# Kernel tuning notes

Hardware: AMD Instinct MI355X
Metric: run time of the kernel (lower is better)

## Reference

```python
import jax, jax.numpy as jnp
import numpy as np

N = 20000   # nodes per type per hop
E = 200000  # edges per relation per hop
H = 512     # node_feature_hid_len
FU = 512    # raw user feature len
FI = 256    # raw item feature len
NUM_RES = 2
NUM_DNN = 2


def setup_inputs() -> dict:
    key = jax.random.key(0)
    ks = iter(jax.random.split(key, 64))
    p = lambda shape: jax.random.normal(next(ks), shape, dtype=jnp.float32) * 0.05
    inp = {}
    # features per hop per type
    for h in range(3):
        inp[f'feat_user_h{h}'] = jax.random.normal(next(ks), (N, FU), dtype=jnp.float32)
        inp[f'feat_item_h{h}'] = jax.random.normal(next(ks), (N, FI), dtype=jnp.float32)
    del inp['feat_user_h2_']; 


def _unused():
    pass

# rebuild setup_inputs cleanly (above stub replaced)

def setup_inputs() -> dict:
    key = jax.random.key(0)
    ks = iter(jax.random.split(key, 64))
    p = lambda shape: jax.random.normal(next(ks), shape, dtype=jnp.float32) * 0.05
    inp = {}
    for h in range(3):
        inp[f'feat_user_h{h}'] = jax.random.normal(next(ks), (N, FU), dtype=jnp.float32)
        inp[f'feat_item_h{h}'] = jax.random.normal(next(ks), (N, FI), dtype=jnp.float32)
    for name in ('edges_UI_h0', 'edges_IU_h0', 'edges_UI_h1', 'edges_IU_h1'):
        inp[name] = jax.random.randint(next(ks), (2, E), 0, N, dtype=jnp.int32)
    # per-node-type input transforms
    inp['W_user'] = p((FU, H)); inp['b_user'] = jnp.zeros((H,), jnp.float32)
    inp['W_item'] = p((FI, H)); inp['b_item'] = jnp.zeros((H,), jnp.float32)
    # per-relation GATConv params, stacked over 2 relations [UI, IU]
    inp['gat_feat_W'] = p((2, H, H)); inp['gat_feat_b'] = jnp.zeros((2, H), jnp.float32)
    inp['gat_att_w'] = p((2, 2 * H)); inp['gat_att_b'] = jnp.zeros((2,), jnp.float32)
    inp['gat_bias'] = jnp.zeros((2, H), jnp.float32)
    # Res_DNN params
    inp['prep_W'] = p((H, H)); inp['prep_b'] = jnp.zeros((H,), jnp.float32)
    inp['dnn_W'] = p((NUM_RES, NUM_DNN, H, H)); inp['dnn_b'] = jnp.zeros((NUM_RES, NUM_DNN, H), jnp.float32)
    inp['dnn_ln_g'] = jnp.ones((NUM_RES, NUM_DNN, H), jnp.float32); inp['dnn_ln_b'] = jnp.zeros((NUM_RES, NUM_DNN, H), jnp.float32)
    inp['res_ln_g'] = jnp.ones((NUM_RES, H), jnp.float32); inp['res_ln_b'] = jnp.zeros((NUM_RES, H), jnp.float32)
    inp['cls_W'] = p((H, 1)); inp['cls_b'] = jnp.zeros((1,), jnp.float32)
    return inp


def _ln(x, g, b, eps=1e-5):
    mu = jnp.mean(x, axis=-1, keepdims=True)
    var = jnp.mean((x - mu) ** 2, axis=-1, keepdims=True)
    return (x - mu) * jax.lax.rsqrt(var + eps) * g + b


def _gat(head_h, tail_h, edges, fW, fb, aw, ab, bias):
    # GATConv: feat_linear on both sides, tanh edge attention, per-source-row
    # sparse softmax, scatter-weighted sum of transformed tail features.
    s = head_h @ fW + fb            # [Nh, H]
    t = tail_h @ fW + fb            # [Nt, H]
    src, tgt = edges[0], edges[1]
    # att(cat([s_e, t_e])) split into per-node scores (same math as concat @ aw)
    e = jnp.tanh((s @ aw[:H])[src] + (t @ aw[H:])[tgt] + ab)  # [E]
    nh = head_h.shape[0]
    m = jax.ops.segment_max(e, src, num_segments=nh)
    ex = jnp.exp(e - m[src])
    den = jax.ops.segment_sum(ex, src, num_segments=nh)
    alpha = ex / den[src]
    hp = jax.ops.segment_sum(alpha[:, None] * t[tgt], src, num_segments=nh)
    return hp + bias


def _forward(feat_user_h0, feat_item_h0, feat_user_h1, feat_item_h1,
             feat_user_h2, feat_item_h2,
             W_user, b_user, W_item, b_item,
             gat_feat_W, gat_feat_b, gat_att_w, gat_att_b, gat_bias,
             prep_W, prep_b, dnn_W, dnn_b, dnn_ln_g, dnn_ln_b,
             res_ln_g, res_ln_b, cls_W, cls_b,
             edges_UI_h0, edges_IU_h0, edges_UI_h1, edges_IU_h1):
    def gat(r, head, tail, edges):
        return _gat(head, tail, edges, gat_feat_W[r], gat_feat_b[r],
                    gat_att_w[r], gat_att_b[r], gat_bias[r])
    # hop 2 (deepest): transformed source features
    su = feat_user_h2 @ W_user + b_user
    si = feat_item_h2 @ W_item + b_item
    # hop 1
    hu = feat_user_h1 @ W_user + b_user
    hi = feat_item_h1 @ W_item + b_item
    su_new = (hu + gat(0, hu, si, edges_UI_h1)) * 0.5  # mean of [self, UI agg]
    si_new = (hi + gat(1, hi, su, edges_IU_h1)) * 0.5
    su, si = su_new, si_new
    # hop 0
    hu = feat_user_h0 @ W_user + b_user
    hi = feat_item_h0 @ W_item + b_item
    su_new = (hu + gat(0, hu, si, edges_UI_h0)) * 0.5
    su = su_new  # target node type = 'user' (first key)
    # Res_DNN head
    x = su @ prep_W + prep_b
    for r in range(NUM_RES):
        sc = x
        for d in range(NUM_DNN):
            x = _ln(jnp.tanh(x @ dnn_W[r, d] + dnn_b[r, d]), dnn_ln_g[r, d], dnn_ln_b[r, d])
        x = _ln(jnp.tanh(sc + x), res_ln_g[r], res_ln_b[r])
    return jax.nn.sigmoid(x @ cls_W + cls_b)  # [N, 1]


def reference(feat_user_h0, feat_item_h0, feat_user_h1, feat_item_h1,
              feat_user_h2, feat_item_h2,
              edges_UI_h0, edges_IU_h0, edges_UI_h1, edges_IU_h1,
              W_user, b_user, W_item, b_item,
              gat_feat_W, gat_feat_b, gat_att_w, gat_att_b, gat_bias,
              prep_W, prep_b, dnn_W, dnn_b, dnn_ln_g, dnn_ln_b,
              res_ln_g, res_ln_b, cls_W, cls_b):
    return _forward(feat_user_h0, feat_item_h0, feat_user_h1, feat_item_h1,
                    feat_user_h2, feat_item_h2,
                    W_user, b_user, W_item, b_item,
                    gat_feat_W, gat_feat_b, gat_att_w, gat_att_b, gat_bias,
                    prep_W, prep_b, dnn_W, dnn_b, dnn_ln_g, dnn_ln_b,
                    res_ln_g, res_ln_b, cls_W, cls_b,
                    edges_UI_h0, edges_IU_h0, edges_UI_h1, edges_IU_h1)
```

## Files before the change

kernel.cpp:

```cpp
#include <hip/hip_runtime.h>
#include <math.h>

#define NN 20000
#define NE 200000
#define HH 512

typedef __attribute__((ext_vector_type(8))) short short8v;
typedef __attribute__((ext_vector_type(4))) float f32x4;

__device__ inline short f2bf(float f) {
    union { float f; unsigned u; } v; v.f = f;
    unsigned r = (v.u + 0x7fffu + ((v.u >> 16) & 1u)) >> 16;
    return (short)r;
}
__device__ inline float bf2f(short s) {
    union { unsigned u; float f; } v;
    v.u = ((unsigned)(unsigned short)s) << 16;
    return v.f;
}

__device__ inline void gload_lds16(const void* g, void* l) {
    __builtin_amdgcn_global_load_lds(
        (const __attribute__((address_space(1))) void*)g,
        (__attribute__((address_space(3))) void*)l, 16, 0, 0);
}

__global__ __launch_bounds__(256)
void f2b_kernel(const float* __restrict__ src, short* __restrict__ dst, int n8)
{
    int i = blockIdx.x * 256 + threadIdx.x;
    if (i >= n8) return;
    const float4* p = (const float4*)src + (size_t)i * 2;
    float4 a = p[0], b = p[1];
    short8v s;
    s[0] = f2bf(a.x); s[1] = f2bf(a.y); s[2] = f2bf(a.z); s[3] = f2bf(a.w);
    s[4] = f2bf(b.x); s[5] = f2bf(b.y); s[6] = f2bf(b.z); s[7] = f2bf(b.w);
    ((short8v*)dst)[i] = s;
}

__global__ __launch_bounds__(256)
void wtr_kernel(const float* __restrict__ src, short* __restrict__ dst,
                int K, int Ncols)
{
    __shared__ float t[32][33];
    int bx = blockIdx.x * 32;
    int by = blockIdx.y * 32;
    int tx = threadIdx.x, ty = threadIdx.y;
    for (int i = ty; i < 32; i += 8)
        t[i][tx] = src[(size_t)(by + i) * Ncols + bx + tx];
    __syncthreads();
    for (int i = ty; i < 32; i += 8)
        dst[(size_t)(bx + i) * K + by + tx] = f2bf(t[tx][i]);
}

__global__ __launch_bounds__(256)
void mfma_lin(const short* __restrict__ X, const short* __restrict__ WT,
              const float* __restrict__ bias, float* __restrict__ outF,
              short* __restrict__ outB, int M, int K)
{
    __shared__ short8v As[2][512];
    __shared__ short8v Bs[2][512];

    const int tid = threadIdx.x;
    const int lane = tid & 63;
    const int w = tid >> 6;

    const int nby = (M + 127) >> 7;
    const int nwg = nby << 2;
    const int q = nwg >> 3, r = nwg & 7;
    int id = blockIdx.x;
    int xcd = id & 7, wi = id >> 3;
    int wgid = (xcd < r ? xcd * (q + 1) : r * (q + 1) + (xcd - r) * q) + wi;
    const int col0 = (wgid & 3) * 128;
    const int row0 = (wgid >> 2) * 128;

    const int wr = (w >> 1) * 64;
    const int wc = (w & 1) * 64;

    int sp0 = w * 128 + lane;
    int sp1 = sp0 + 64;
    int r0_ = sp0 >> 2, r1_ = sp1 >> 2;
    int c0_ = (sp0 & 3) ^ ((r0_ >> 1) & 3);
    int c1_ = (sp1 & 3) ^ ((r1_ >> 1) & 3);
    int ga0 = row0 + r0_; if (ga0 >= M) ga0 = M - 1;
    int ga1 = row0 + r1_; if (ga1 >= M) ga1 = M - 1;
    const short* ag0 = X + (size_t)ga0 * K + c0_ * 8;
    const short* ag1 = X + (size_t)ga1 * K + c1_ * 8;
    const short* bg0 = WT + (size_t)(col0 + r0_) * K + c0_ * 8;
    const short* bg1 = WT + (size_t)(col0 + r1_) * K + c1_ * 8;

    int ar[4], br[4];
#pragma unroll
    for (int i = 0; i < 4; ++i) {
        int rr = wr + i * 16 + (lane & 15);
        ar[i] = rr * 4 + ((lane >> 4) ^ ((rr >> 1) & 3));
        int nn = wc + i * 16 + (lane & 15);
        br[i] = nn * 4 + ((lane >> 4) ^ ((nn >> 1) & 3));
    }

    f32x4 acc[4][4];
#pragma unroll
    for (int i = 0; i < 4; ++i)
#pragma unroll
        for (int j = 0; j < 4; ++j)
            acc[i][j] = (f32x4){0.f, 0.f, 0.f, 0.f};

    auto stage = [&](int buf, int kk) {
        gload_lds16(ag0 + kk, &As[buf][sp0 & ~63]);
        gload_lds16(ag1 + kk, &As[buf][sp1 & ~63]);
        gload_lds16(bg0 + kk, &Bs[buf][sp0 & ~63]);
        gload_lds16(bg1 + kk, &Bs[buf][sp1 & ~63]);
    };

    const int nt = K >> 5;
    stage(0, 0);
    __syncthreads();
    int cur = 0;
    for (int t = 0; t < nt; ++t) {
        if (t + 1 < nt) stage(cur ^ 1, (t + 1) * 32);
        short8v af[4], bf[4];
#pragma unroll
        for (int i = 0; i < 4; ++i) af[i] = As[cur][ar[i]];
#pragma unroll
        for (int j = 0; j < 4; ++j) bf[j] = Bs[cur][br[j]];
#pragma unroll
        for (int i = 0; i < 4; ++i)
#pragma unroll
            for (int j = 0; j < 4; ++j)
                acc[i][j] = __builtin_amdgcn_mfma_f32_16x16x32_bf16(af[i], bf[j], acc[i][j], 0, 0, 0);
        __syncthreads();
        cur ^= 1;
    }

    float bj[4];
#pragma unroll
    for (int j = 0; j < 4; ++j)
        bj[j] = bias[col0 + wc + j * 16 + (lane & 15)];
#pragma unroll
    for (int i = 0; i < 4; ++i) {
#pragma unroll
        for (int rr = 0; rr < 4; ++rr) {
            int row = row0 + wr + i * 16 + (lane >> 4) * 4 + rr;
            if (row < M) {
                size_t base = (size_t)row * HH + col0 + wc + (lane & 15);
                if (outF) {
                    float* op = outF + base;
#pragma unroll
                    for (int j = 0; j < 4; ++j) op[j * 16] = acc[i][j][rr] + bj[j];
                }
                if (outB) {
                    short* op = outB + base;
#pragma unroll
                    for (int j = 0; j < 4; ++j) op[j * 16] = f2bf(acc[i][j][rr] + bj[j]);
                }
            }
        }
    }
}

__global__ __launch_bounds__(256)
void gat_pre_kernel(const float* __restrict__ fW, const float* __restrict__ fb,
                    const float* __restrict__ aw, float* __restrict__ uv,
                    float* __restrict__ s0t0)
{
    int row = blockIdx.x * 4 + (threadIdx.x >> 6);
    int lane = threadIdx.x & 63;
    const float4* ah = (const float4*)aw;
    const float4* at = (const float4*)(aw + HH);
    const float4* fp;
    if (row < 512)      fp = (const float4*)(fW + (size_t)row * HH);
    else if (row == 512) fp = (const float4*)fb;
    else return;
    float du = 0.f, dv = 0.f;
#pragma unroll
    for (int l = 0; l < 2; ++l) {
        int idx = lane * 2 + l;
        float4 f = fp[idx], a = ah[idx], b = at[idx];
        du += f.x*a.x + f.y*a.y + f.z*a.z + f.w*a.w;
        dv += f.x*b.x + f.y*b.y + f.z*b.z + f.w*b.w;
    }
#pragma unroll
    for (int m = 32; m >= 1; m >>= 1) {
        du += __shfl_xor(du, m);
        dv += __shfl_xor(dv, m);
    }
    if (lane == 0) {
        if (row < 512) { uv[row] = du; uv[512 + row] = dv; }
        else           { s0t0[0] = du; s0t0[1] = dv; }
    }
}

__global__ __launch_bounds__(256)
void rowdot2_kernel(const short* __restrict__ Hd, const short* __restrict__ Tl,
                    const float* __restrict__ uv, const float* __restrict__ s0t0,
                    float* __restrict__ ss, float* __restrict__ ts, int N)
{
    int row = blockIdx.x * 4 + (threadIdx.x >> 6);
    int lane = threadIdx.x & 63;
    if (row >= N) return;
    short8v h = ((const short8v*)(Hd + (size_t)row * HH))[lane];
    short8v t = ((const short8v*)(Tl + (size_t)row * HH))[lane];
    const float4* up = (const float4*)uv + lane * 2;
    const float4* vp = (const float4*)(uv + HH) + lane * 2;
    float4 u0 = up[0], u1 = up[1], v0 = vp[0], v1 = vp[1];
    float a = bf2f(h[0])*u0.x + bf2f(h[1])*u0.y + bf2f(h[2])*u0.z + bf2f(h[3])*u0.w
            + bf2f(h[4])*u1.x + bf2f(h[5])*u1.y + bf2f(h[6])*u1.z + bf2f(h[7])*u1.w;
    float b = bf2f(t[0])*v0.x + bf2f(t[1])*v0.y + bf2f(t[2])*v0.z + bf2f(t[3])*v0.w
            + bf2f(t[4])*v1.x + bf2f(t[5])*v1.y + bf2f(t[6])*v1.z + bf2f(t[7])*v1.w;
#pragma unroll
    for (int m = 32; m >= 1; m >>= 1) {
        a += __shfl_xor(a, m);
        b += __shfl_xor(b, m);
    }
    if (lane == 0) { ss[row] = a + s0t0[0]; ts[row] = b + s0t0[1]; }
}

__global__ __launch_bounds__(256)
void count2_kernel(const int* __restrict__ s0, const int* __restrict__ s1,
                   int* __restrict__ c0, int* __restrict__ c1, int E)
{
    int i = blockIdx.x * blockDim.x + threadIdx.x;
    if (i < E) atomicAdd(&c0[s0[i]], 1);
    else if (i < 2 * E) atomicAdd(&c1[s1[i - E]], 1);
}

__global__ __launch_bounds__(1024)
void scan2_kernel(const int* __restrict__ c0, const int* __restrict__ c1,
                  int* __restrict__ o0, int* __restrict__ o1,
                  int* __restrict__ u0, int* __restrict__ u1, int n)
{
    const int* counts = blockIdx.x ? c1 : c0;
    int* offs = blockIdx.x ? o1 : o0;
    int* curs = blockIdx.x ? u1 : u0;
    __shared__ int part[1024];
    const int tid = threadIdx.x;
    const int CH = (n + 1023) / 1024;
    const int base = tid * CH;
    int s = 0;
    for (int i = 0; i < CH; ++i) {
        int idx = base + i;
        if (idx < n) s += counts[idx];
    }
    part[tid] = s;
    __syncthreads();
    for (int d = 1; d < 1024; d <<= 1) {
        int v = 0;
        if (tid >= d) v = part[tid - d];
        __syncthreads();
        if (tid >= d) part[tid] += v;
        __syncthreads();
    }
    int run = (tid == 0) ? 0 : part[tid - 1];
    for (int i = 0; i < CH; ++i) {
        int idx = base + i;
        if (idx < n) { offs[idx] = run; curs[idx] = run; run += counts[idx]; }
    }
    if (tid == 1023) offs[n] = run;
}

__global__ __launch_bounds__(256)
void fill_kernel(const int* __restrict__ src, const int* __restrict__ tgt,
                 const float* __restrict__ ss, const float* __restrict__ ts,
                 const float* __restrict__ ab_ptr, int* __restrict__ cursor,
                 int* __restrict__ tvals, float* __restrict__ wv, int E)
{
    int i = blockIdx.x * blockDim.x + threadIdx.x;
    if (i >= E) return;
    int s = src[i], t = tgt[i];
    int pos = atomicAdd(&cursor[s], 1);
    tvals[pos] = t;
    wv[pos] = expf(tanhf(ss[s] + ts[t] + ab_ptr[0]));
}

__global__ __launch_bounds__(256)
void gat_agg_kernel(const int* __restrict__ offs, const int* __restrict__ tvals,
                    const float* __restrict__ wv, const short* __restrict__ T,
                    const short* __restrict__ head, const float* __restrict__ gbias,
                    short* __restrict__ out, int N)
{
    int s = blockIdx.x * 4 + (threadIdx.x >> 6);
    int lane = threadIdx.x & 63;
    if (s >= N) return;
    const int beg = offs[s], end = offs[s + 1];
    float a[8];
#pragma unroll
    for (int q = 0; q < 8; ++q) a[q] = 0.f;
    float den = 0.f;

    int j = beg;
    float wq = 0.f; short8v tvq;
    if (j < end) {
        wq = wv[j];
        tvq = ((const short8v*)(T + (size_t)tvals[j] * HH))[lane];
    }
    while (j < end) {
        float w = wq; short8v tv = tvq;
        ++j;
        if (j < end) {
            wq = wv[j];
            tvq = ((const short8v*)(T + (size_t)tvals[j] * HH))[lane];
        }
        den += w;
#pragma unroll
        for (int q = 0; q < 8; ++q) a[q] = fmaf(w, bf2f(tv[q]), a[q]);
    }
    float inv = (den > 0.f) ? 1.f / den : 0.f;

    short8v h = ((const short8v*)(head + (size_t)s * HH))[lane];
    const float4* bp = (const float4*)gbias + lane * 2;
    float4 b0 = bp[0], b1 = bp[1];
    float bb[8] = {b0.x, b0.y, b0.z, b0.w, b1.x, b1.y, b1.z, b1.w};
    short8v o;
#pragma unroll
    for (int q = 0; q < 8; ++q)
        o[q] = f2bf((bf2f(h[q]) + a[q] * inv + bb[q]) * 0.5f);
    ((short8v*)(out + (size_t)s * HH))[lane] = o;
}

__global__ __launch_bounds__(256)
void tanh_ln_kernel(const short* __restrict__ Z, const float* __restrict__ res,
                    const float* __restrict__ g, const float* __restrict__ bta,
                    short* __restrict__ outB, float* __restrict__ outF,
                    const float* __restrict__ cWp, const float* __restrict__ cbp,
                    float* __restrict__ outCls, int N)
{
    int row = blockIdx.x * 4 + (threadIdx.x >> 6);
    int lane = threadIdx.x & 63;
    if (row >= N) return;
    short8v zv = ((const short8v*)(Z + (size_t)row * HH))[lane];
    float v[8];
    float sum = 0.f, sum2 = 0.f;
    float rr[8];
    if (res) {
        const float4* rp = (const float4*)(res + (size_t)row * HH) + lane * 2;
        float4 r0 = rp[0], r1 = rp[1];
        rr[0]=r0.x; rr[1]=r0.y; rr[2]=r0.z; rr[3]=r0.w;
        rr[4]=r1.x; rr[5]=r1.y; rr[6]=r1.z; rr[7]=r1.w;
    } else {
#pragma unroll
        for (int q = 0; q < 8; ++q) rr[q] = 0.f;
    }
#pragma unroll
    for (int q = 0; q < 8; ++q) {
        float t = tanhf(bf2f(zv[q]) + rr[q]);
        v[q] = t;
        sum += t;
        sum2 = fmaf(t, t, sum2);
    }
#pragma unroll
    for (int m = 32; m >= 1; m >>= 1) {
        sum  += __shfl_xor(sum, m);
        sum2 += __shfl_xor(sum2, m);
    }
    float mu  = sum * (1.f/HH);
    float var = sum2 * (1.f/HH) - mu*mu;
    float rs  = rsqrtf(var + 1e-5f);
    const float4* gp = (const float4*)g + lane * 2;
    const float4* bp = (const float4*)bta + lane * 2;
    float4 g0 = gp[0], g1 = gp[1], c0 = bp[0], c1 = bp[1];
    float gg[8] = {g0.x, g0.y, g0.z, g0.w, g1.x, g1.y, g1.z, g1.w};
    float cc[8] = {c0.x, c0.y, c0.z, c0.w, c1.x, c1.y, c1.z, c1.w};
    float o[8];
#pragma unroll
    for (int q = 0; q < 8; ++q) o[q] = (v[q]-mu)*rs*gg[q] + cc[q];
    if (outB) {
        short8v ob;
#pragma unroll
        for (int q = 0; q < 8; ++q) ob[q] = f2bf(o[q]);
        ((short8v*)(outB + (size_t)row * HH))[lane] = ob;
    }
    if (outF) {
        float4* op = (float4*)(outF + (size_t)row * HH) + lane * 2;
        op[0] = make_float4(o[0], o[1], o[2], o[3]);
        op[1] = make_float4(o[4], o[5], o[6], o[7]);
    }
    if (cWp) {
        const float4* wp = (const float4*)cWp + lane * 2;
        float4 w0 = wp[0], w1 = wp[1];
        float acc = o[0]*w0.x + o[1]*w0.y + o[2]*w0.z + o[3]*w0.w
                  + o[4]*w1.x + o[5]*w1.y + o[6]*w1.z + o[7]*w1.w;
#pragma unroll
        for (int m = 32; m >= 1; m >>= 1) acc += __shfl_xor(acc, m);
        if (lane == 0) outCls[row] = 1.f / (1.f + expf(-(acc + cbp[0])));
    }
}

extern "C" void kernel_launch(void* const* d_in, const int* in_sizes, int n_in,
                              void* d_out, int out_size, void* d_ws, size_t ws_size,
                              hipStream_t stream)
{
    (void)in_sizes; (void)n_in; (void)out_size; (void)ws_size;
    const int N = NN, E = NE, H = HH;
    const size_t NHf = (size_t)N * H;

    const float* fu0 = (const float*)d_in[0];
    const float* fi1 = (const float*)d_in[3];
    const float* fu2 = (const float*)d_in[4];
    const int* eUI0 = (const int*)d_in[6];
    const int* eIU1 = (const int*)d_in[9];
    const float* Wu  = (const float*)d_in[10];
    const float* bu  = (const float*)d_in[11];
    const float* Wi  = (const float*)d_in[12];
    const float* bi  = (const float*)d_in[13];
    const float* gfW = (const float*)d_in[14];
    const float* gfb = (const float*)d_in[15];
    const float* gaw = (const float*)d_in[16];
    const float* gab = (const float*)d_in[17];
    const float* gbias = (const float*)d_in[18];
    const float* prW = (const float*)d_in[19];
    const float* prb = (const float*)d_in[20];
    const float* dW  = (const float*)d_in[21];
    const float* db  = (const float*)d_in[22];
    const float* dlg = (const float*)d_in[23];
    const float* dlb = (const float*)d_in[24];
    const float* rlg = (const float*)d_in[25];
    const float* rlb = (const float*)d_in[26];
    const float* cW  = (const float*)d_in[27];
    const float* cb  = (const float*)d_in[28];

    float* B5   = (float*)d_ws;
    float* ssb  = B5 + NHf;
    float* tsb  = ssb + N;
    float* uv   = tsb + N;
    float* s0t0 = uv + 1024;
    float* wvb  = s0t0 + 4;
    int* counts0 = (int*)(wvb + E);
    int* counts1 = counts0 + N;
    int* offs0   = counts1 + N;
    int* offs1   = offs0 + N + 1;
    int* cur0    = offs1 + N + 1;
    int* cur1    = cur0 + N;
    int* tvals   = cur1 + N;
    size_t boff = (size_t)((char*)(tvals + E) - (char*)d_ws);
    boff = (boff + 15) & ~(size_t)15;
    short* S0    = (short*)((char*)d_ws + boff);
    short* XI1   = S0 + NHf;
    short* SU    = XI1 + NHf / 2;
    short* HI    = SU + NHf;
    short* SINEW = HI + NHf;
    short* T4    = SINEW + NHf;
    short* SUF   = T4 + NHf;
    short* WTu   = SUF + NHf;
    short* WTi   = WTu + 512 * 512;
    short* WTg0  = WTi + 512 * 256;
    short* WTg1  = WTg0 + 512 * 512;
    short* WTpr  = WTg1 + 512 * 512;
    short* WTd   = WTpr + 512 * 512;
    short* XU0 = S0;
    short* HU0 = HI;
    short* XB  = SINEW;
    short* ZB  = SU;

    auto WTR = [&](const float* src, short* dst, int K) {
        hipLaunchKernelGGL(wtr_kernel, dim3(16, K / 32), dim3(32, 8), 0, stream,
                           src, dst, K, 512);
    };
    WTR(Wu, WTu, 512);
    WTR(Wi, WTi, 256);
    WTR(gfW, WTg0, 512);
    WTR(gfW + (size_t)H * H, WTg1, 512);
    WTR(prW, WTpr, 512);
    for (int k = 0; k < 4; ++k)
        WTR(dW + (size_t)k * H * H, WTd + (size_t)k * 512 * 512, 512);

    auto F2B = [&](const float* src, short* dst, size_t n) {
        int n8 = (int)(n / 8);
        hipLaunchKernelGGL(f2b_kernel, dim3((n8 + 255) / 256), dim3(256), 0, stream,
                           src, dst, n8);
    };

    hipMemsetAsync(counts0, 0, 2 * N * sizeof(int), stream);
    hipLaunchKernelGGL(count2_kernel, dim3((2 * E + 255) / 256), dim3(256), 0, stream,
                       eUI0, eIU1, counts0, counts1, E);
    hipLaunchKernelGGL(scan2_kernel, dim3(2), dim3(1024), 0, stream,
                       counts0, counts1, offs0, offs1, cur0, cur1, N);

    const int nby = (N + 127) / 128;
    const int nwg = nby * 4;
    auto MLIN = [&](const short* X, const short* WT, const float* b,
                    float* oF, short* oB, int K) {
        hipLaunchKernelGGL(mfma_lin, dim3(nwg), dim3(256), 0, stream,
                           X, WT, b, oF, oB, N, K);
    };
    const int rgrid = (N + 3) / 4;
    const int egrid = (E + 255) / 256;

    auto GAT = [&](int r, const short* headB, const short* tailB, const short* WTg,
                   const int* edges, int* offs, int* curs, short* outB) {
        hipLaunchKernelGGL(gat_pre_kernel, dim3(130), dim3(256), 0, stream,
                           gfW + (size_t)r * H * H, gfb + r * H, gaw + (size_t)r * 2 * H,
                           uv, s0t0);
        MLIN(tailB, WTg, gfb + r * H, nullptr, T4, 512);
        hipLaunchKernelGGL(rowdot2_kernel, dim3(rgrid), dim3(256), 0, stream,
                           headB, tailB, uv, s0t0, ssb, tsb, N);
        hipLaunchKernelGGL(fill_kernel, dim3(egrid), dim3(256), 0, stream,
                           edges, edges + E, ssb, tsb, gab + r, curs, tvals, wvb, E);
        hipLaunchKernelGGL(gat_agg_kernel, dim3(rgrid), dim3(256), 0, stream,
                           offs, tvals, wvb, T4, headB, gbias + (size_t)r * H, outB, N);
    };

    F2B(fu2, S0, NHf);
    F2B(fi1, XI1, NHf / 2);
    MLIN(S0, WTu, bu, nullptr, SU, 512);
    MLIN(XI1, WTi, bi, nullptr, HI, 256);
    GAT(1, HI, SU, WTg1, eIU1, offs1, cur1, SINEW);
    F2B(fu0, XU0, NHf);
    MLIN(XU0, WTu, bu, nullptr, HU0, 512);
    GAT(0, HU0, SINEW, WTg0, eUI0, offs0, cur0, SUF);

    MLIN(SUF, WTpr, prb, B5, XB, 512);
    for (int r = 0; r < 2; ++r) {
        for (int d = 0; d < 2; ++d) {
            MLIN(XB, WTd + (size_t)(r * 2 + d) * 512 * 512, db + (r * 2 + d) * H,
                 nullptr, ZB, 512);
            hipLaunchKernelGGL(tanh_ln_kernel, dim3(rgrid), dim3(256), 0, stream,
                               ZB, (const float*)nullptr, dlg + (r * 2 + d) * H,
                               dlb + (r * 2 + d) * H, XB, (float*)nullptr,
                               (const float*)nullptr, (const float*)nullptr,
                               (float*)nullptr, N);
        }
        if (r == 0) {
            hipLaunchKernelGGL(tanh_ln_kernel, dim3(rgrid), dim3(256), 0, stream,
                               XB, B5, rlg, rlb, XB, B5,
                               (const float*)nullptr, (const float*)nullptr,
                               (float*)nullptr, N);
        } else {
            hipLaunchKernelGGL(tanh_ln_kernel, dim3(rgrid), dim3(256), 0, stream,
                               XB, B5, rlg + H, rlb + H, (short*)nullptr,
                               (float*)nullptr, cW, cb, (float*)d_out, N);
        }
    }
}
```

Baseline: 594.7 us.

## Fuse DNN GEMMs with tanh/layernorm epilogues, batch user transforms, unroll GAT aggregation

Adds an MFMA kernel computing a full 512-wide row tile of 32 rows, so the tanh, layernorm, residual tanh-layernorm and final classifier sigmoid are applied in the epilogue instead of separate elementwise kernels. The two user feature transforms share one GEMM over 2N rows, and the GAT aggregation loop issues four gathers per iteration. This removes intermediate bf16 round trips and several launches, but the small 32-row tile reloads the whole weight matrix per block, reducing operand reuse.

Result: slower. 719.8 us (+21.0%).

```diff
diff --git a/kernel.cpp b/kernel.cpp
--- a/kernel.cpp
+++ b/kernel.cpp
@@ -154,6 +154,280 @@
                     for (int j = 0; j < 4; ++j) op[j * 16] = f2bf(acc[i][j][rr] + bj[j]);
                 }
             }
+        }
+    }
+}
+
+__global__ __launch_bounds__(256)
+void mfma_dnn(const short* __restrict__ X, const short* __restrict__ WT,
+              const float* __restrict__ bias,
+              const float* __restrict__ g1, const float* __restrict__ b1,
+              const float* __restrict__ scp,
+              const float* __restrict__ g2, const float* __restrict__ b2,
+              short* __restrict__ outB, float* __restrict__ outF,
+              const float* __restrict__ cWp, const float* __restrict__ cbp,
+              float* __restrict__ outCls, int M)
+{
+    __shared__ short8v As[128];
+    __shared__ short8v Bs[2048];
+    __shared__ float red[4][32][2];
+    __shared__ float lnp[32][2];
+
+    const int tid = threadIdx.x;
+    const int lane = tid & 63;
+    const int w = tid >> 6;
+
+    const int nwg = M >> 5;
+    const int q = nwg >> 3, r = nwg & 7;
+    int id = blockIdx.x;
+    int xcd = id & 7, wi = id >> 3;
+    int wgid = (xcd < r ? xcd * (q + 1) : r * (q + 1) + (xcd - r) * q) + wi;
+    const int row0 = wgid * 32;
+
+    const int bslotbase = w * 512;
+    const short* bgp[8];
+#pragma unroll
+    for (int g = 0; g < 8; ++g) {
+        int p = bslotbase + g * 64 + lane;
+        int col = p >> 2;
+        int ch = (p & 3) ^ ((col >> 1) & 3);
+        bgp[g] = WT + (size_t)col * HH + ch * 8;
+    }
+    const short* agp[2];
+    if (w == 0) {
+#pragma unroll
+        for (int g = 0; g < 2; ++g) {
+            int p = g * 64 + lane;
+            int row = p >> 2;
+            int ch = (p & 3) ^ ((row >> 1) & 3);
+            agp[g] = X + (size_t)(row0 + row) * HH + ch * 8;
+        }
+    }
+
+    int afr[2], bfr[8];
+#pragma unroll
+    for (int i = 0; i < 2; ++i) {
+        int rw = i * 16 + (lane & 15);
+        afr[i] = rw * 4 + ((lane >> 4) ^ ((rw >> 1) & 3));
+    }
+#pragma unroll
+    for (int j = 0; j < 8; ++j) {
+        int cc = w * 128 + j * 16 + (lane & 15);
+        bfr[j] = cc * 4 + ((lane >> 4) ^ ((cc >> 1) & 3));
+    }
+
+    f32x4 acc[2][8];
+#pragma unroll
+    for (int i = 0; i < 2; ++i)
+#pragma unroll
+        for (int j = 0; j < 8; ++j)
+            acc[i][j] = (f32x4){0.f, 0.f, 0.f, 0.f};
+
+    for (int t = 0; t < 16; ++t) {
+        int kk = t * 32;
+#pragma unroll
+        for (int g = 0; g < 8; ++g)
+            gload_lds16(bgp[g] + kk, &Bs[bslotbase + g * 64]);
+        if (w == 0) {
+#pragma unroll
+            for (int g = 0; g < 2; ++g)
+                gload_lds16(agp[g] + kk, &As[g * 64]);
+        }
+        __syncthreads();
+        short8v af[2], bf[8];
+#pragma unroll
+        for (int i = 0; i < 2; ++i) af[i] = As[afr[i]];
+#pragma unroll
+        for (int j = 0; j < 8; ++j) bf[j] = Bs[bfr[j]];
+#pragma unroll
+        for (int i = 0; i < 2; ++i)
+#pragma unroll
+            for (int j = 0; j < 8; ++j)
+                acc[i][j] = __builtin_amdgcn_mfma_f32_16x16x32_bf16(af[i], bf[j], acc[i][j], 0, 0, 0);
+        __syncthreads();
+    }
+
+    const int colb = w * 128 + (lane & 15);
+    float bj[8], g1j[8], b1j[8];
+#pragma unroll
+    for (int j = 0; j < 8; ++j) {
+        bj[j]  = bias[colb + j * 16];
+        g1j[j] = g1[colb + j * 16];
+        b1j[j] = b1[colb + j * 16];
+    }
+#pragma unroll
+    for (int i = 0; i < 2; ++i)
+#pragma unroll
+        for (int j = 0; j < 8; ++j)
+#pragma unroll
+            for (int rr = 0; rr < 4; ++rr)
+                acc[i][j][rr] = tanhf(acc[i][j][rr] + bj[j]);
+
+    {
+        float s1[2][4], s2[2][4];
+#pragma unroll
+        for (int i = 0; i < 2; ++i)
+#pragma unroll
+            for (int rr = 0; rr < 4; ++rr) {
+                float s = 0.f, ss = 0.f;
+#pragma unroll
+                for (int j = 0; j < 8; ++j) {
+                    float v = acc[i][j][rr];
+                    s += v; ss = fmaf(v, v, ss);
+                }
+#pragma unroll
+                for (int m = 1; m <= 8; m <<= 1) {
+                    s += __shfl_xor(s, m); ss += __shfl_xor(ss, m);
+                }
+                s1[i][rr] = s; s2[i][rr] = ss;
+            }
+        if ((lane & 15) == 0) {
+#pragma unroll
+            for (int i = 0; i < 2; ++i)
+#pragma unroll
+                for (int rr = 0; rr < 4; ++rr) {
+                    int row = i * 16 + (lane >> 4) * 4 + rr;
+                    red[w][row][0] = s1[i][rr];
+                    red[w][row][1] = s2[i][rr];
+                }
+        }
+        __syncthreads();
+        if (tid < 32) {
+            float s = red[0][tid][0] + red[1][tid][0] + red[2][tid][0] + red[3][tid][0];
+            float ss = red[0][tid][1] + red[1][tid][1] + red[2][tid][1] + red[3][tid][1];
+            float mu = s * (1.f / HH);
+            float var = ss * (1.f / HH) - mu * mu;
+            lnp[tid][0] = mu; lnp[tid][1] = rsqrtf(var + 1e-5f);
+        }
+        __syncthreads();
+    }
+#pragma unroll
+    for (int i = 0; i < 2; ++i)
+#pragma unroll
+        for (int rr = 0; rr < 4; ++rr) {
+            int row = i * 16 + (lane >> 4) * 4 + rr;
+            float mu = lnp[row][0], rs = lnp[row][1];
+#pragma unroll
+            for (int j = 0; j < 8; ++j)
+                acc[i][j][rr] = (acc[i][j][rr] - mu) * rs * g1j[j] + b1j[j];
+        }
+
+    if (scp) {
+#pragma unroll
+        for (int i = 0; i < 2; ++i)
+#pragma unroll
+            for (int rr = 0; rr < 4; ++rr) {
+                int row = i * 16 + (lane >> 4) * 4 + rr;
+                const float* sp = scp + (size_t)(row0 + row) * HH;
+#pragma unroll
+                for (int j = 0; j < 8; ++j)
+                    acc[i][j][rr] = tanhf(sp[colb + j * 16] + acc[i][j][rr]);
+            }
+        __syncthreads();
+        float s1[2][4], s2[2][4];
+#pragma unroll
+        for (int i = 0; i < 2; ++i)
+#pragma unroll
+            for (int rr = 0; rr < 4; ++rr) {
+                float s = 0.f, ss = 0.f;
+#pragma unroll
+                for (int j = 0; j < 8; ++j) {
+                    float v = acc[i][j][rr];
+                    s += v; ss = fmaf(v, v, ss);
+                }
+#pragma unroll
+                for (int m = 1; m <= 8; m <<= 1) {
+                    s += __shfl_xor(s, m); ss += __shfl_xor(ss, m);
+                }
+                s1[i][rr] = s; s2[i][rr] = ss;
+            }
+        if ((lane & 15) == 0) {
+#pragma unroll
+            for (int i = 0; i < 2; ++i)
+#pragma unroll
+                for (int rr = 0; rr < 4; ++rr) {
+                    int row = i * 16 + (lane >> 4) * 4 + rr;
+                    red[w][row][0] = s1[i][rr];
+                    red[w][row][1] = s2[i][rr];
+                }
+        }
+        __syncthreads();
+        if (tid < 32) {
+            float s = red[0][tid][0] + red[1][tid][0] + red[2][tid][0] + red[3][tid][0];
+            float ss = red[0][tid][1] + red[1][tid][1] + red[2][tid][1] + red[3][tid][1];
+            float mu = s * (1.f / HH);
+            float var = ss * (1.f / HH) - mu * mu;
+            lnp[tid][0] = mu; lnp[tid][1] = rsqrtf(var + 1e-5f);
+        }
+        __syncthreads();
+        float g2j[8], b2j[8];
+#pragma unroll
+        for (int j = 0; j < 8; ++j) {
+            g2j[j] = g2[colb + j * 16];
+            b2j[j] = b2[colb + j * 16];
+        }
+#pragma unroll
+        for (int i = 0; i < 2; ++i)
+#pragma unroll
+            for (int rr = 0; rr < 4; ++rr) {
+                int row = i * 16 + (lane >> 4) * 4 + rr;
+                float mu = lnp[row][0], rs = lnp[row][1];
+#pragma unroll
+                for (int j = 0; j < 8; ++j)
+                    acc[i][j][rr] = (acc[i][j][rr] - mu) * rs * g2j[j] + b2j[j];
+            }
+    }
+
+    if (outB) {
+#pragma unroll
+        for (int i = 0; i < 2; ++i)
+#pragma unroll
+            for (int rr = 0; rr < 4; ++rr) {
+                int row = row0 + i * 16 + (lane >> 4) * 4 + rr;
+                short* op = outB + (size_t)row * HH + colb;
+#pragma unroll
+                for (int j = 0; j < 8; ++j) op[j * 16] = f2bf(acc[i][j][rr]);
+            }
+    }
+    if (outF) {
+#pragma unroll
+        for (int i = 0; i < 2; ++i)
+#pragma unroll
+            for (int rr = 0; rr < 4; ++rr) {
+                int row = row0 + i * 16 + (lane >> 4) * 4 + rr;
+                float* op = outF + (size_t)row * HH + colb;
+#pragma unroll
+                for (int j = 0; j < 8; ++j) op[j * 16] = acc[i][j][rr];
+            }
+    }
+    if (cWp) {
+        float cw[8];
+#pragma unroll
+        for (int j = 0; j < 8; ++j) cw[j] = cWp[colb + j * 16];
+        __syncthreads();
+        float d[2][4];
+#pragma unroll
+        for (int i = 0; i < 2; ++i)
+#pragma unroll
+            for (int rr = 0; rr < 4; ++rr) {
+                float s = 0.f;
+#pragma unroll
+                for (int j = 0; j < 8; ++j) s = fmaf(acc[i][j][rr], cw[j], s);
+#pragma unroll
+                for (int m = 1; m <= 8; m <<= 1) s += __shfl_xor(s, m);
+                d[i][rr] = s;
+            }
+        if ((lane & 15) == 0) {
+#pragma unroll
+            for (int i = 0; i < 2; ++i)
+#pragma unroll
+                for (int rr = 0; rr < 4; ++rr)
+                    red[w][i * 16 + (lane >> 4) * 4 + rr][0] = d[i][rr];
+        }
+        __syncthreads();
+        if (tid < 32) {
+            float s = red[0][tid][0] + red[1][tid][0] + red[2][tid][0] + red[3][tid][0];
+            outCls[row0 + tid] = 1.f / (1.f + expf(-(s + cbp[0])));
         }
     }
 }
@@ -288,18 +562,28 @@
     float den = 0.f;
 
     int j = beg;
-    float wq = 0.f; short8v tvq;
-    if (j < end) {
-        wq = wv[j];
-        tvq = ((const short8v*)(T + (size_t)tvals[j] * HH))[lane];
-    }
-    while (j < end) {
-        float w = wq; short8v tv = tvq;
-        ++j;
-        if (j < end) {
-            wq = wv[j];
-            tvq = ((const short8v*)(T + (size_t)tvals[j] * HH))[lane];
-        }
+    for (; j + 4 <= end; j += 4) {
+        int t0 = tvals[j], t1 = tvals[j + 1], t2 = tvals[j + 2], t3 = tvals[j + 3];
+        float w0 = wv[j], w1 = wv[j + 1], w2 = wv[j + 2], w3 = wv[j + 3];
+        short8v v0 = ((const short8v*)(T + (size_t)t0 * HH))[lane];
+        short8v v1 = ((const short8v*)(T + (size_t)t1 * HH))[lane];
+        short8v v2 = ((const short8v*)(T + (size_t)t2 * HH))[lane];
+        short8v v3 = ((const short8v*)(T + (size_t)t3 * HH))[lane];
+        den += w0 + w1 + w2 + w3;
+#pragma unroll
+        for (int q = 0; q < 8; ++q) {
+            float acc = a[q];
+            acc = fmaf(w0, bf2f(v0[q]), acc);
+            acc = fmaf(w1, bf2f(v1[q]), acc);
+            acc = fmaf(w2, bf2f(v2[q]), acc);
+            acc = fmaf(w3, bf2f(v3[q]), acc);
+            a[q] = acc;
+        }
+    }
+    for (; j < end; ++j) {
+        int t = tvals[j];
+        float w = wv[j];
+        short8v tv = ((const short8v*)(T + (size_t)t * HH))[lane];
         den += w;
 #pragma unroll
         for (int q = 0; q < 8; ++q) a[q] = fmaf(w, bf2f(tv[q]), a[q]);
@@ -315,74 +599,6 @@
     for (int q = 0; q < 8; ++q)
         o[q] = f2bf((bf2f(h[q]) + a[q] * inv + bb[q]) * 0.5f);
     ((short8v*)(out + (size_t)s * HH))[lane] = o;
-}
-
-__global__ __launch_bounds__(256)
-void tanh_ln_kernel(const short* __restrict__ Z, const float* __restrict__ res,
-                    const float* __restrict__ g, const float* __restrict__ bta,
-                    short* __restrict__ outB, float* __restrict__ outF,
-                    const float* __restrict__ cWp, const float* __restrict__ cbp,
-                    float* __restrict__ outCls, int N)
-{
-    int row = blockIdx.x * 4 + (threadIdx.x >> 6);
-    int lane = threadIdx.x & 63;
-    if (row >= N) return;
-    short8v zv = ((const short8v*)(Z + (size_t)row * HH))[lane];
-    float v[8];
-    float sum = 0.f, sum2 = 0.f;
-    float rr[8];
-    if (res) {
-        const float4* rp = (const float4*)(res + (size_t)row * HH) + lane * 2;
-        float4 r0 = rp[0], r1 = rp[1];
-        rr[0]=r0.x; rr[1]=r0.y; rr[2]=r0.z; rr[3]=r0.w;
-        rr[4]=r1.x; rr[5]=r1.y; rr[6]=r1.z; rr[7]=r1.w;
-    } else {
-#pragma unroll
-        for (int q = 0; q < 8; ++q) rr[q] = 0.f;
-    }
-#pragma unroll
-    for (int q = 0; q < 8; ++q) {
-        float t = tanhf(bf2f(zv[q]) + rr[q]);
-        v[q] = t;
-        sum += t;
-        sum2 = fmaf(t, t, sum2);
-    }
-#pragma unroll
-    for (int m = 32; m >= 1; m >>= 1) {
-        sum  += __shfl_xor(sum, m);
-        sum2 += __shfl_xor(sum2, m);
-    }
-    float mu  = sum * (1.f/HH);
-    float var = sum2 * (1.f/HH) - mu*mu;
-    float rs  = rsqrtf(var + 1e-5f);
-    const float4* gp = (const float4*)g + lane * 2;
-    const float4* bp = (const float4*)bta + lane * 2;
-    float4 g0 = gp[0], g1 = gp[1], c0 = bp[0], c1 = bp[1];
-    float gg[8] = {g0.x, g0.y, g0.z, g0.w, g1.x, g1.y, g1.z, g1.w};
-    float cc[8] = {c0.x, c0.y, c0.z, c0.w, c1.x, c1.y, c1.z, c1.w};
-    float o[8];
-#pragma unroll
-    for (int q = 0; q < 8; ++q) o[q] = (v[q]-mu)*rs*gg[q] + cc[q];
-    if (outB) {
-        short8v ob;
-#pragma unroll
-        for (int q = 0; q < 8; ++q) ob[q] = f2bf(o[q]);
-        ((short8v*)(outB + (size_t)row * HH))[lane] = ob;
-    }
-    if (outF) {
-        float4* op = (float4*)(outF + (size_t)row * HH) + lane * 2;
-        op[0] = make_float4(o[0], o[1], o[2], o[3]);
-        op[1] = make_float4(o[4], o[5], o[6], o[7]);
-    }
-    if (cWp) {
-        const float4* wp = (const float4*)cWp + lane * 2;
-        float4 w0 = wp[0], w1 = wp[1];
-        float acc = o[0]*w0.x + o[1]*w0.y + o[2]*w0.z + o[3]*w0.w
-                  + o[4]*w1.x + o[5]*w1.y + o[6]*w1.z + o[7]*w1.w;
-#pragma unroll
-        for (int m = 32; m >= 1; m >>= 1) acc += __shfl_xor(acc, m);
-        if (lane == 0) outCls[row] = 1.f / (1.f + expf(-(acc + cbp[0])));
-    }
 }
 
 extern "C" void kernel_launch(void* const* d_in, const int* in_sizes, int n_in,
@@ -434,9 +650,9 @@
     size_t boff = (size_t)((char*)(tvals + E) - (char*)d_ws);
     boff = (boff + 15) & ~(size_t)15;
     short* S0    = (short*)((char*)d_ws + boff);
-    short* XI1   = S0 + NHf;
-    short* SU    = XI1 + NHf / 2;
-    short* HI    = SU + NHf;
+    short* SUHU  = S0 + 2 * NHf;
+    short* XI1   = SUHU + 2 * NHf;
+    short* HI    = XI1 + NHf / 2;
     short* SINEW = HI + NHf;
     short* T4    = SINEW + NHf;
     short* SUF   = T4 + NHf;
@@ -446,10 +662,9 @@
     short* WTg1  = WTg0 + 512 * 512;
     short* WTpr  = WTg1 + 512 * 512;
     short* WTd   = WTpr + 512 * 512;
-    short* XU0 = S0;
-    short* HU0 = HI;
+    short* SU  = SUHU;
+    short* HU0 = SUHU + NHf;
     short* XB  = SINEW;
-    short* ZB  = SU;
 
     auto WTR = [&](const float* src, short* dst, int K) {
         hipLaunchKernelGGL(wtr_kernel, dim3(16, K / 32), dim3(32, 8), 0, stream,
@@ -475,12 +690,11 @@
     hipLaunchKernelGGL(scan2_kernel, dim3(2), dim3(1024), 0, stream,
                        counts0, counts1, offs0, offs1, cur0, cur1, N);
 
-    const int nby = (N + 127) / 128;
-    const int nwg = nby * 4;
     auto MLIN = [&](const short* X, const short* WT, const float* b,
-                    float* oF, short* oB, int K) {
+                    float* oF, short* oB, int M, int K) {
+        int nwg = ((M + 127) / 128) * 4;
         hipLaunchKernelGGL(mfma_lin, dim3(nwg), dim3(256), 0, stream,
-                           X, WT, b, oF, oB, N, K);
+                           X, WT, b, oF, oB, M, K);
     };
     const int rgrid = (N + 3) / 4;
     const int egrid = (E + 255) / 256;
@@ -490,7 +704,7 @@
         hipLaunchKernelGGL(gat_pre_kernel, dim3(130), dim3(256), 0, stream,
                            gfW + (size_t)r * H * H, gfb + r * H, gaw + (size_t)r * 2 * H,
                            uv, s0t0);
-        MLIN(tailB, WTg, gfb + r * H, nullptr, T4, 512);
+        MLIN(tailB, WTg, gfb + r * H, nullptr, T4, N, 512);
         hipLaunchKernelGGL(rowdot2_kernel, dim3(rgrid), dim3(256), 0, stream,
                            headB, tailB, uv, s0t0, ssb, tsb, N);
         hipLaunchKernelGGL(fill_kernel, dim3(egrid), dim3(256), 0, stream,
@@ -500,34 +714,33 @@
     };
 
     F2B(fu2, S0, NHf);
+    F2B(fu0, S0 + NHf, NHf);
     F2B(fi1, XI1, NHf / 2);
-    MLIN(S0, WTu, bu, nullptr, SU, 512);
-    MLIN(XI1, WTi, bi, nullptr, HI, 256);
+    MLIN(S0, WTu, bu, nullptr, SUHU, 2 * N, 512);
+    MLIN(XI1, WTi, bi, nullptr, HI, N, 256);
     GAT(1, HI, SU, WTg1, eIU1, offs1, cur1, SINEW);
-    F2B(fu0, XU0, NHf);
-    MLIN(XU0, WTu, bu, nullptr, HU0, 512);
     GAT(0, HU0, SINEW, WTg0, eUI0, offs0, cur0, SUF);
 
-    MLIN(SUF, WTpr, prb, B5, XB, 512);
-    for (int r = 0; r < 2; ++r) {
-        for (int d = 0; d < 2; ++d) {
-            MLIN(XB, WTd + (size_t)(r * 2 + d) * 512 * 512, db + (r * 2 + d) * H,
-                 nullptr, ZB, 512);
-            hipLaunchKernelGGL(tanh_ln_kernel, dim3(rgrid), dim3(256), 0, stream,
-                               ZB, (const float*)nullptr, dlg + (r * 2 + d) * H,
-                               dlb + (r * 2 + d) * H, XB, (float*)nullptr,
-                               (const float*)nullptr, (const float*)nullptr,
-                               (float*)nullptr, N);
-        }
-        if (r == 0) {
-            hipLaunchKernelGGL(tanh_ln_kernel, dim3(rgrid), dim3(256), 0, stream,
-                               XB, B5, rlg, rlb, XB, B5,
-                               (const float*)nullptr, (const float*)nullptr,
-                               (float*)nullptr, N);
-        } else {
-            hipLaunchKernelGGL(tanh_ln_kernel, dim3(rgrid), dim3(256), 0, stream,
-                               XB, B5, rlg + H, rlb + H, (short*)nullptr,
-                               (float*)nullptr, cW, cb, (float*)d_out, N);
-        }
-    }
-}
+    MLIN(SUF, WTpr, prb, B5, XB, N, 512);
+    const int dgrid = N / 32;
+    hipLaunchKernelGGL(mfma_dnn, dim3(dgrid), dim3(256), 0, stream,
+                       XB, WTd, db, dlg, dlb,
+                       (const float*)nullptr, (const float*)nullptr, (const float*)nullptr,
+                       XB, (float*)nullptr,
+                       (const float*)nullptr, (const float*)nullptr, (float*)nullptr, N);
+    hipLaunchKernelGGL(mfma_dnn, dim3(dgrid), dim3(256), 0, stream,
+                       XB, WTd + (size_t)1 * 512 * 512, db + H, dlg + H, dlb + H,
+                       B5, rlg, rlb,
+                       XB, B5,
+                       (const float*)nullptr, (const float*)nullptr, (float*)nullptr, N);
+    hipLaunchKernelGGL(mfma_dnn, dim3(dgrid), dim3(256), 0, stream,
+                       XB, WTd + (size_t)2 * 512 * 512, db + 2 * H, dlg + 2 * H, dlb + 2 * H,
+                       (const float*)nullptr, (const float*)nullptr, (const float*)nullptr,
+                       XB, (float*)nullptr,
+                       (const float*)nullptr, (const float*)nullptr, (float*)nullptr, N);
+    hipLaunchKernelGGL(mfma_dnn, dim3(dgrid), dim3(256), 0, stream,
+                       XB, WTd + (size_t)3 * 512 * 512, db + 3 * H, dlg + 3 * H, dlb + 3 * H,
+                       B5, rlg + H, rlb + H,
+                       (short*)nullptr, (float*)nullptr,
+                       cW, cb, (float*)d_out, N);
+}
```
